# Performance work log

Hardware: AMD Instinct MI355X
Metric: run time of the kernel (lower is better)

## Reference

```python
import jax, jax.numpy as jnp
import numpy as np

NQ = 4
DEPTH = 6
_PAIRS = [(0, 1), (0, 2), (0, 3), (1, 2), (1, 3), (2, 3)]


def _z_signs():
    # sign table (16, 10): columns = [Z0..Z3, Z0Z1, Z0Z2, Z0Z3, Z1Z2, Z1Z3, Z2Z3]
    # wire 0 is the most-significant bit (PennyLane convention)
    bits = (np.arange(16)[:, None] >> np.arange(NQ - 1, -1, -1)[None, :]) & 1
    z = 1.0 - 2.0 * bits  # (16, 4)
    cols = [z[:, i] for i in range(NQ)] + [z[:, i] * z[:, j] for i, j in _PAIRS]
    return np.stack(cols, axis=1).astype(np.float32)  # (16, 10)

_ZSIGNS = jnp.asarray(_z_signs())


def _apply_1q(state, U, q):
    # state: (B, 2,2,2,2); apply 2x2 U on qubit axis 1+q
    s = jnp.moveaxis(state, 1 + q, -1)
    s = jnp.einsum('...j,ij->...i', s, U)
    return jnp.moveaxis(s, -1, 1 + q)


def _cnot(state, c, t):
    a0 = jax.lax.index_in_dim(state, 0, axis=1 + c, keepdims=True)
    a1 = jax.lax.index_in_dim(state, 1, axis=1 + c, keepdims=True)
    a1 = jnp.flip(a1, axis=1 + t)
    return jnp.concatenate([a0, a1], axis=1 + c)


def _circuit(amps, weights):
    # amps: (B, 16) real unit vectors; weights: (DEPTH, NQ)
    B = amps.shape[0]
    psi = amps.astype(jnp.complex64).reshape(B, 2, 2, 2, 2)
    for l in range(DEPTH):
        for q in range(NQ):
            half = weights[l, q] * 0.5
            c = jnp.cos(half).astype(jnp.complex64)
            s = (-1j) * jnp.sin(half).astype(jnp.complex64)
            U = jnp.stack([jnp.stack([c, s]), jnp.stack([s, c])])  # RX gate
            psi = _apply_1q(psi, U, q)
        for q in range(NQ):  # CNOT ring
            psi = _cnot(psi, q, (q + 1) % NQ)
    return psi.reshape(B, 16)


def setup_inputs() -> dict:
    key = jax.random.key(0)
    kx, kw, kh = jax.random.split(key, 3)
    x = jax.random.normal(kx, (8192, 1, 64, 64), dtype=jnp.float32)
    q_weights = jax.random.uniform(kw, (DEPTH, NQ), dtype=jnp.float32, maxval=2.0 * np.pi)
    head_w = jax.random.normal(kh, (10, 10), dtype=jnp.float32) * 0.1
    head_b = jnp.zeros((10,), dtype=jnp.float32)
    scale = jnp.asarray(3.0, dtype=jnp.float32)
    return {"x": x, "q_weights": q_weights, "head_w": head_w, "head_b": head_b, "scale": scale}


def reference(x, q_weights, head_w, head_b, scale):
    B, _, H, W = x.shape
    # adaptive_avg_pool2d to (4,4): average over (H/4, W/4) blocks
    pooled = x.reshape(B, 1, 4, H // 4, 4, W // 4).mean(axis=(3, 5))  # (B,1,4,4)
    v = pooled.reshape(B, 16)
    amps = v / jnp.linalg.norm(v, axis=1, keepdims=True)  # AmplitudeEmbedding(normalize=True)
    psi = _circuit(amps, q_weights)  # (B, 16) complex
    probs = psi.real ** 2 + psi.imag ** 2  # (B, 16)
    feats = probs @ _ZSIGNS  # (B, 10): <Z_i> and <Z_i Z_j>
    out = feats @ head_w.T + head_b
    return out * scale
```

## Files before the change

### kernel.cpp

```cpp
#include <hip/hip_runtime.h>


#define QNET_NQ 4
#define QNET_DEPTH 6

__global__ __launch_bounds__(256) void qnet_kernel(
    const float* __restrict__ x,
    const float* __restrict__ qw,
    const float* __restrict__ head_w,
    const float* __restrict__ head_b,
    const float* __restrict__ scale,
    float* __restrict__ out)
{
    const int b    = blockIdx.x;
    const int t    = threadIdx.x;
    const int wave = t >> 6;
    const int lane = t & 63;

    __shared__ float pooled[16];

    const float* img = x + (size_t)b * 4096 + (size_t)wave * 1024;
    float s = 0.f;
#pragma unroll
    for (int i = 0; i < 4; ++i) {
        float4 v = *reinterpret_cast<const float4*>(img + 4 * (lane + 64 * i));
        s += v.x + v.y + v.z + v.w;
    }
    s += __shfl_xor(s, 32);
    s += __shfl_xor(s, 16);
    s += __shfl_xor(s, 2);
    s += __shfl_xor(s, 1);
    if (lane < 16 && (lane & 3) == 0)
        pooled[wave * 4 + (lane >> 2)] = s * (1.0f / 256.0f);
    __syncthreads();

    if (wave != 0) return;

    const int idx = lane & 15;
    float v  = pooled[idx];
    float n2 = v * v;
    n2 += __shfl_xor(n2, 1);
    n2 += __shfl_xor(n2, 2);
    n2 += __shfl_xor(n2, 4);
    n2 += __shfl_xor(n2, 8);
    const float inv = rsqrtf(n2);
    float re = v * inv;
    float im = 0.f;

#pragma unroll
    for (int l = 0; l < QNET_DEPTH; ++l) {
#pragma unroll
        for (int q = 0; q < QNET_NQ; ++q) {
            const float half = 0.5f * qw[l * QNET_NQ + q];
            float sn, cs;
            sincosf(half, &sn, &cs);
            const int bit = 1 << (3 - q);
            const float re_p = __shfl_xor(re, bit);
            const float im_p = __shfl_xor(im, bit);
            re = cs * re + sn * im_p;
            im = cs * im - sn * re_p;
        }
#pragma unroll
        for (int q = 0; q < QNET_NQ; ++q) {
            const int cb = 1 << (3 - q);
            const int tb = 1 << (3 - ((q + 1) & 3));
            const float re_s = __shfl_xor(re, tb);
            const float im_s = __shfl_xor(im, tb);
            const bool ctrl = (idx & cb) != 0;
            re = ctrl ? re_s : re;
            im = ctrl ? im_s : im;
        }
    }

    const float prob = re * re + im * im;

    const int r = (lane < 10) ? lane : 0;
    float hw[10];
#pragma unroll
    for (int k = 0; k < 10; ++k) hw[k] = head_w[r * 10 + k];

    float acc = head_b[r];
#pragma unroll
    for (int i2 = 0; i2 < 16; ++i2) {
        const float p  = __shfl(prob, i2);
        const float z0 = (i2 & 8) ? -1.f : 1.f;
        const float z1 = (i2 & 4) ? -1.f : 1.f;
        const float z2 = (i2 & 2) ? -1.f : 1.f;
        const float z3 = (i2 & 1) ? -1.f : 1.f;
        const float m = z0 * hw[0] + z1 * hw[1] + z2 * hw[2] + z3 * hw[3]
                      + (z0 * z1) * hw[4] + (z0 * z2) * hw[5] + (z0 * z3) * hw[6]
                      + (z1 * z2) * hw[7] + (z1 * z3) * hw[8] + (z2 * z3) * hw[9];
        acc += p * m;
    }
    if (lane < 10)
        out[(size_t)b * 10 + lane] = acc * scale[0];
}

extern "C" void kernel_launch(void* const* d_in, const int* in_sizes, int n_in,
                              void* d_out, int out_size, void* d_ws, size_t ws_size,
                              hipStream_t stream) {
    const float* x      = (const float*)d_in[0];
    const float* qw     = (const float*)d_in[1];
    const float* head_w = (const float*)d_in[2];
    const float* head_b = (const float*)d_in[3];
    const float* scale  = (const float*)d_in[4];
    float* out = (float*)d_out;

    const int B = in_sizes[0] / 4096;
    qnet_kernel<<<B, 256, 0, stream>>>(x, qw, head_w, head_b, scale, out);
}
```

Baseline: 195.5 us.

## Precompute circuit unitary and head matrix in a setup kernel

```diff
diff --git a/kernel.cpp b/kernel.cpp
--- a/kernel.cpp
+++ b/kernel.cpp
@@ -4,49 +4,17 @@
 #define QNET_NQ 4
 #define QNET_DEPTH 6
 
-__global__ __launch_bounds__(256) void qnet_kernel(
-    const float* __restrict__ x,
+__global__ __launch_bounds__(256) void qnet_tables(
     const float* __restrict__ qw,
     const float* __restrict__ head_w,
-    const float* __restrict__ head_b,
-    const float* __restrict__ scale,
-    float* __restrict__ out)
+    float* __restrict__ tab)
 {
-    const int b    = blockIdx.x;
-    const int t    = threadIdx.x;
-    const int wave = t >> 6;
-    const int lane = t & 63;
+    const int t   = threadIdx.x;
+    const int k   = t >> 4;
+    const int idx = t & 15;
 
-    __shared__ float pooled[16];
-
-    const float* img = x + (size_t)b * 4096 + (size_t)wave * 1024;
-    float s = 0.f;
-#pragma unroll
-    for (int i = 0; i < 4; ++i) {
-        float4 v = *reinterpret_cast<const float4*>(img + 4 * (lane + 64 * i));
-        s += v.x + v.y + v.z + v.w;
-    }
-    s += __shfl_xor(s, 32);
-    s += __shfl_xor(s, 16);
-    s += __shfl_xor(s, 2);
-    s += __shfl_xor(s, 1);
-    if (lane < 16 && (lane & 3) == 0)
-        pooled[wave * 4 + (lane >> 2)] = s * (1.0f / 256.0f);
-    __syncthreads();
-
-    if (wave != 0) return;
-
-    const int idx = lane & 15;
-    float v  = pooled[idx];
-    float n2 = v * v;
-    n2 += __shfl_xor(n2, 1);
-    n2 += __shfl_xor(n2, 2);
-    n2 += __shfl_xor(n2, 4);
-    n2 += __shfl_xor(n2, 8);
-    const float inv = rsqrtf(n2);
-    float re = v * inv;
+    float re = (idx == k) ? 1.f : 0.f;
     float im = 0.f;
-
 #pragma unroll
     for (int l = 0; l < QNET_DEPTH; ++l) {
 #pragma unroll
@@ -71,29 +39,76 @@
             im = ctrl ? im_s : im;
         }
     }
+    tab[idx * 16 + k]       = re;
+    tab[256 + idx * 16 + k] = im;
 
-    const float prob = re * re + im * im;
+    if (t < 160) {
+        const int r = t >> 4, j = t & 15;
+        const float z0 = (j & 8) ? -1.f : 1.f;
+        const float z1 = (j & 4) ? -1.f : 1.f;
+        const float z2 = (j & 2) ? -1.f : 1.f;
+        const float z3 = (j & 1) ? -1.f : 1.f;
+        const float* hw = head_w + r * 10;
+        tab[512 + t] = z0 * hw[0] + z1 * hw[1] + z2 * hw[2] + z3 * hw[3]
+                     + (z0 * z1) * hw[4] + (z0 * z2) * hw[5] + (z0 * z3) * hw[6]
+                     + (z1 * z2) * hw[7] + (z1 * z3) * hw[8] + (z2 * z3) * hw[9];
+    }
+}
+
+__global__ __launch_bounds__(256) void qnet_main(
+    const float* __restrict__ x,
+    const float* __restrict__ tab,
+    const float* __restrict__ head_b,
+    const float* __restrict__ scale,
+    float* __restrict__ out)
+{
+    __shared__ float pooled[16];
+    __shared__ float ltab[672];
+
+    const int b    = blockIdx.x;
+    const int t    = threadIdx.x;
+    const int wave = t >> 6;
+    const int lane = t & 63;
+
+    for (int i = t; i < 672; i += 256) ltab[i] = tab[i];
+
+    const float* img = x + (size_t)b * 4096 + (size_t)wave * 1024;
+    float s = 0.f;
+#pragma unroll
+    for (int i = 0; i < 4; ++i) {
+        float4 v = *reinterpret_cast<const float4*>(img + 4 * (lane + 64 * i));
+        s += v.x + v.y + v.z + v.w;
+    }
+    s += __shfl_xor(s, 32);
+    s += __shfl_xor(s, 16);
+    s += __shfl_xor(s, 2);
+    s += __shfl_xor(s, 1);
+    if (lane < 16 && (lane & 3) == 0)
+        pooled[wave * 4 + (lane >> 2)] = s * (1.0f / 256.0f);
+    __syncthreads();
+
+    if (wave != 0) return;
+
+    const int j = lane & 15;
+    float sre = 0.f, sim = 0.f, n2 = 0.f;
+#pragma unroll
+    for (int k = 0; k < 16; ++k) {
+        const float a = pooled[k];
+        n2  = fmaf(a, a, n2);
+        sre = fmaf(ltab[j * 16 + k], a, sre);
+        sim = fmaf(ltab[256 + j * 16 + k], a, sim);
+    }
+    const float prob = (sre * sre + sim * sim) / n2;
 
     const int r = (lane < 10) ? lane : 0;
-    float hw[10];
+    float acc = 0.f;
 #pragma unroll
-    for (int k = 0; k < 10; ++k) hw[k] = head_w[r * 10 + k];
-
-    float acc = head_b[r];
-#pragma unroll
-    for (int i2 = 0; i2 < 16; ++i2) {
-        const float p  = __shfl(prob, i2);
-        const float z0 = (i2 & 8) ? -1.f : 1.f;
-        const float z1 = (i2 & 4) ? -1.f : 1.f;
-        const float z2 = (i2 & 2) ? -1.f : 1.f;
-        const float z3 = (i2 & 1) ? -1.f : 1.f;
-        const float m = z0 * hw[0] + z1 * hw[1] + z2 * hw[2] + z3 * hw[3]
-                      + (z0 * z1) * hw[4] + (z0 * z2) * hw[5] + (z0 * z3) * hw[6]
-                      + (z1 * z2) * hw[7] + (z1 * z3) * hw[8] + (z2 * z3) * hw[9];
-        acc += p * m;
+    for (int jj = 0; jj < 16; ++jj) {
+        const float p = __shfl(prob, jj);
+        acc = fmaf(ltab[512 + r * 16 + jj], p, acc);
     }
     if (lane < 10)
-        out[(size_t)b * 10 + lane] = acc * scale[0];
+        out[(size_t)b * 10 + lane] = (head_b[lane] + acc) * scale[0];
 }
 
 extern "C" void kernel_launch(void* const* d_in, const int* in_sizes, int n_in,
@@ -105,7 +120,10 @@
     const float* head_b = (const float*)d_in[3];
     const float* scale  = (const float*)d_in[4];
     float* out = (float*)d_out;
+    float* tab = (float*)d_ws;
 
     const int B = in_sizes[0] / 4096;
-    qnet_kernel<<<B, 256, 0, stream>>>(x, qw, head_w, head_b, scale, out);
+
+    qnet_tables<<<1, 256, 0, stream>>>(qw, head_w, tab);
+    qnet_main<<<B, 256, 0, stream>>>(x, tab, head_b, scale, out);
 }
```

Result: no change. 199.1 us (+1.9%).
